# Optimization experiments

Measured on AMD Instinct MI355X. Metric: run time of the kernel, lower is better.

The kernel has to match this reference:

```python
import jax, jax.numpy as jnp
import numpy as np


def setup_inputs() -> dict:
    key = jax.random.key(0)
    k1, k2, k3 = jax.random.split(key, 3)
    Q, N, D = 2048, 100000, 512
    x = jax.random.normal(k1, (Q, D), dtype=jnp.float32)
    target_embeddings = jax.random.normal(k2, (N, D), dtype=jnp.float32)
    target_labels = jax.random.randint(k3, (N,), 0, 400, dtype=jnp.int64)
    return {"x": x, "target_embeddings": target_embeddings,
            "target_labels": target_labels, "k": 5}


def reference(x, target_embeddings, target_labels, k):
    # torch.cdist(x[:,None], T[None], p=2).squeeze(1): full [Q, N] euclidean distances
    x2 = jnp.sum(x * x, axis=-1, keepdims=True)            # [Q, 1]
    t2 = jnp.sum(target_embeddings * target_embeddings, axis=-1)  # [N]
    d2 = x2 + t2[None, :] - 2.0 * (x @ target_embeddings.T)       # [Q, N]
    dist = jnp.sqrt(jnp.maximum(d2, 0.0))
    # topk smallest distances
    neg_vals, topk_inds = jax.lax.top_k(-dist, k)           # [Q, k]
    topk_dists = -neg_vals
    # pred = target_labels[inds].t() in the original eval path
    pred = target_labels[topk_inds].T                       # [k, Q]
    return topk_dists, topk_inds, pred
```

## Files before the change

### kernel.cpp

```cpp
#include <hip/hip_runtime.h>
#include <hip/hip_fp8.h>
#include <float.h>
#include <math.h>

#define NQ 2048
#define NT 100000
#define DIM 512
#define KTOP 5
#define NCAND 16
#define QTILE 128
#define TTILE 128
#define NTPC 13
#define NCH 64
#define TBLKS 782
#define QBLKS 16
#define NSUB 3
#define CV_TBLKS (TBLKS*16)
#define CV_XBLKS ((NQ/128)*16)

typedef float f32x4 __attribute__((ext_vector_type(4)));
typedef unsigned int u32;
typedef unsigned short u16;
typedef unsigned long u64;

__device__ __forceinline__ int tsub_start(int ts) { return (13 * ts + 2) / 3; }

__device__ __forceinline__ bool lt_pair(float v1, int i1, float v2, int i2) {
  return v1 < v2 || (v1 == v2 && i1 < i2);
}

__device__ __forceinline__ void ins5f(float* tv, int* tix, float sc, int idx) {
  if (sc < tv[4]) {
    tv[4] = sc; tix[4] = idx;
#pragma unroll
    for (int p = 4; p > 0; --p)
      if (tv[p] < tv[p - 1]) {
        float tf = tv[p]; tv[p] = tv[p - 1]; tv[p - 1] = tf;
        int tn = tix[p]; tix[p] = tix[p - 1]; tix[p - 1] = tn;
      }
  }
}

__device__ __forceinline__ void ins5(float* tv, int* tix, float sc, int idx) {
  if (lt_pair(sc, idx, tv[4], tix[4])) {
    tv[4] = sc; tix[4] = idx;
#pragma unroll
    for (int p = 4; p > 0; --p)
      if (lt_pair(tv[p], tix[p], tv[p - 1], tix[p - 1])) {
        float tf = tv[p]; tv[p] = tv[p - 1]; tv[p - 1] = tf;
        int tn = tix[p]; tix[p] = tix[p - 1]; tix[p - 1] = tn;
      }
  }
}

__device__ __forceinline__ void merge5(float* av, int* ai, const float* bv, const int* bi) {
  float nv[5]; int ni[5];
#pragma unroll
  for (int s = 0; s < 5; ++s) {
    if (lt_pair(av[s], ai[s], bv[4 - s], bi[4 - s])) { nv[s] = av[s]; ni[s] = ai[s]; }
    else { nv[s] = bv[4 - s]; ni[s] = bi[4 - s]; }
  }
#pragma unroll
  for (int a = 0; a < 5; ++a)
#pragma unroll
    for (int b = 0; b < 4 - a; ++b)
      if (lt_pair(nv[b + 1], ni[b + 1], nv[b], ni[b])) {
        float tf = nv[b]; nv[b] = nv[b + 1]; nv[b + 1] = tf;
        int tn = ni[b]; ni[b] = ni[b + 1]; ni[b + 1] = tn;
      }
#pragma unroll
  for (int s = 0; s < 5; ++s) { av[s] = nv[s]; ai[s] = ni[s]; }
}

__global__ __launch_bounds__(256) void convert_kernel(
    const float* __restrict__ x, const float* __restrict__ T,
    unsigned char* __restrict__ xq8, unsigned char* __restrict__ tq8,
    float* __restrict__ t2, float* __restrict__ x2) {
  __shared__ unsigned char lh[4096];
  const int bid = blockIdx.x;
  const bool isT = bid < CV_TBLKS;
  const int task = isT ? bid : bid - CV_TBLKS;
  const int blk = task >> 4, kbi = task & 15;
  const float* src = isT ? T : x;
  unsigned char* dq8 = isT ? tq8 : xq8;
  float* nrm = isT ? t2 : x2;
  const int nsrc = isT ? NT : NQ;

  const int t = threadIdx.x;
  const int rr = t >> 1, half = t & 1;
  const int grow = blk * 128 + rr;
  const int rs = grow < nsrc ? grow : nsrc - 1;
  const float* p = src + (size_t)rs * DIM + kbi * 32 + half * 16;
  f32x4 v[4];
#pragma unroll
  for (int i = 0; i < 4; ++i) v[i] = ((const f32x4*)p)[i];

  float ss = 0.f;
#pragma unroll
  for (int g = 0; g < 2; ++g) {
    u64 pk = 0;
#pragma unroll
    for (int e = 0; e < 8; ++e) {
      int i = g * 8 + e;
      float f = v[i >> 2][i & 3];
      ss = fmaf(f, f, ss);
      __hip_fp8_e4m3 q8(f);
      pk |= (u64)__builtin_bit_cast(unsigned char, q8) << (8 * e);
    }
    int unit = (rr >> 4) * 64 + (half * 2 + g) * 16 + (rr & 15);
    *(u64*)(lh + unit * 8) = pk;
  }
  ss += __shfl_xor(ss, 1, 64);
  if (half == 0 && grow < nsrc) atomicAdd(nrm + grow, ss);

  __syncthreads();
  size_t obase = ((size_t)(blk * 16 + kbi)) * 4096 + t * 16;
  *(f32x4*)(dq8 + obase) = *(const f32x4*)(lh + t * 16);
}

__global__ __launch_bounds__(256, 2) void knn_mfma(
    const unsigned char* __restrict__ xq8, const unsigned char* __restrict__ tq8,
    const float* __restrict__ t2g,
    float* __restrict__ pvals, u16* __restrict__ pidx16) {
  __shared__ float msv[128 * 5];
  __shared__ int   msi[128 * 5];

  const int tid = threadIdx.x;
  const int w = tid >> 6;
  const int l = tid & 63;
  const int bid = blockIdx.x;
  const u32 rest = (u32)bid >> 3;
  const int inner = (int)(rest % 48u);
  const int chunk = (bid & 7) + 8 * (int)(rest / 48u);
  const int qblk = inner & 15;
  const int tsub = inner >> 4;
  const int tstart = tsub_start(tsub);
  const int tend = tsub_start(tsub + 1);
  const int q0 = qblk * QTILE;
  const int wr = (w >> 1) * 64;
  const int wc = (w & 1) * 64;
  const int arow = wr >> 4;
  const int bcol = wc >> 4;

  const u64* x64 = (const u64*)xq8;
  const u64* t64 = (const u64*)tq8;

  float tv4[4][KTOP]; int tix4[4][KTOP];
#pragma unroll
  for (int jj = 0; jj < 4; ++jj)
#pragma unroll
    for (int s = 0; s < KTOP; ++s) { tv4[jj][s] = FLT_MAX; tix4[jj][s] = 0x7FFFFFFF; }

#pragma unroll 1
  for (int tt = tstart; tt < tend; ++tt) {
    const int bblk = chunk * NTPC + tt;
    if (bblk >= TBLKS) continue;
    const int tbase = bblk * TTILE;
    f32x4 acc[4][4];
#pragma unroll
    for (int i = 0; i < 4; ++i)
#pragma unroll
      for (int j = 0; j < 4; ++j) acc[i][j] = (f32x4){0.f, 0.f, 0.f, 0.f};

    u32 offA = (u32)(bblk * 16) * 512u + (u32)(arow * 64 + l);
    u32 offB = (u32)(qblk * 16) * 512u + (u32)(bcol * 64 + l);
    long ah[4], bh[4];
#pragma unroll 1
    for (int kbi = 0; kbi < 16; ++kbi) {
#pragma unroll
      for (int i = 0; i < 4; ++i) {
        ah[i] = (long)t64[offA + i * 64];
        bh[i] = (long)x64[offB + i * 64];
      }
      offA += 512; offB += 512;
      __builtin_amdgcn_s_setprio(1);
#pragma unroll
      for (int j = 0; j < 4; ++j)
#pragma unroll
        for (int i = 0; i < 4; ++i)
          acc[i][j] = __builtin_amdgcn_mfma_f32_16x16x32_fp8_fp8(ah[i], bh[j], acc[i][j], 0, 0, 0);
      __builtin_amdgcn_s_setprio(0);
    }

    const int tg0 = tbase + wr + ((l >> 4) << 2);
    float t2v[16];
#pragma unroll
    for (int i = 0; i < 4; ++i)
#pragma unroll
      for (int r = 0; r < 4; ++r) {
        int t = tg0 + i * 16 + r;
        float vv = t2g[t < NT ? t : NT - 1];
        t2v[i * 4 + r] = t < NT ? vv : FLT_MAX;
      }
#pragma unroll
    for (int jj = 0; jj < 4; ++jj)
#pragma unroll
      for (int i = 0; i < 4; ++i)
#pragma unroll
        for (int r = 0; r < 4; ++r) {
          float sc = fmaf(-2.f, acc[i][jj][r], t2v[i * 4 + r]);
          ins5f(tv4[jj], tix4[jj], sc, tg0 + i * 16 + r);
        }
  }

#pragma unroll
  for (int jj = 0; jj < 4; ++jj)
#pragma unroll
    for (int d = 16; d <= 32; d <<= 1) {
      float ov[KTOP]; int oi[KTOP];
#pragma unroll
      for (int s = 0; s < KTOP; ++s) {
        ov[s] = __shfl_xor(tv4[jj][s], d, 64);
        oi[s] = __shfl_xor(tix4[jj][s], d, 64);
      }
      merge5(tv4[jj], tix4[jj], ov, oi);
    }

  const int blockBase = (chunk * NTPC + tstart) * TTILE;
  if ((w >> 1) && (l >> 4) == 0) {
#pragma unroll
    for (int jj = 0; jj < 4; ++jj) {
      int qr = wc + jj * 16 + l;
#pragma unroll
      for (int s = 0; s < KTOP; ++s) {
        msv[qr * 5 + s] = tv4[jj][s];
        msi[qr * 5 + s] = tix4[jj][s];
      }
    }
  }
  __syncthreads();
  if (!(w >> 1) && (l >> 4) == 0) {
#pragma unroll
    for (int jj = 0; jj < 4; ++jj) {
      int qr = wc + jj * 16 + l;
      float ov[KTOP]; int oi[KTOP];
#pragma unroll
      for (int s = 0; s < KTOP; ++s) { ov[s] = msv[qr * 5 + s]; oi[s] = msi[qr * 5 + s]; }
      merge5(tv4[jj], tix4[jj], ov, oi);
      int q = q0 + qr;
      size_t base = ((size_t)q * (NCH * NSUB) + (chunk * NSUB + tsub)) * KTOP;
#pragma unroll
      for (int s = 0; s < KTOP; ++s) {
        pvals[base + s] = tv4[jj][s];
        pidx16[base + s] = (u16)(tix4[jj][s] - blockBase);
      }
    }
  }
}

__global__ __launch_bounds__(256) void knn_merge16(
    const float* __restrict__ pvals, const u16* __restrict__ pidx16,
    int* __restrict__ idx16g) {
  const int M = NCH * NSUB * KTOP;
  int q = (blockIdx.x * 256 + threadIdx.x) >> 6;
  int l = threadIdx.x & 63;
  if (q >= NQ) return;
  float v[15]; int ix[15];
  size_t base = (size_t)q * M;
#pragma unroll
  for (int j = 0; j < 15; ++j) {
    int m = j * 64 + l;
    int slot = m / KTOP;
    int ch = slot / NSUB, ts = slot % NSUB;
    int gb = (ch * NTPC + tsub_start(ts)) * TTILE;
    v[j] = pvals[base + m];
    ix[j] = gb + (int)pidx16[base + m];
  }
  int mywin = 0x7FFFFFFF;
#pragma unroll 1
  for (int r = 0; r < NCAND; ++r) {
    float bv = FLT_MAX; int bi = 0x7FFFFFFF;
#pragma unroll
    for (int j = 0; j < 15; ++j)
      if (lt_pair(v[j], ix[j], bv, bi)) { bv = v[j]; bi = ix[j]; }
#pragma unroll
    for (int d = 1; d < 64; d <<= 1) {
      float ov = __shfl_xor(bv, d, 64);
      int oi = __shfl_xor(bi, d, 64);
      if (lt_pair(ov, oi, bv, bi)) { bv = ov; bi = oi; }
    }
    if (l == r) mywin = bi;
#pragma unroll
    for (int j = 0; j < 15; ++j)
      if (ix[j] == bi) v[j] = FLT_MAX;
  }
  if (l < NCAND) idx16g[q * NCAND + l] = mywin;
}

__global__ __launch_bounds__(256) void knn_rerank(
    const float* __restrict__ x, const float* __restrict__ T,
    const int* __restrict__ idx16g, const int* __restrict__ labels,
    float* __restrict__ out) {
  __shared__ float sd2[4 * NCAND];
  __shared__ int sti[4 * NCAND];
  const int w = threadIdx.x >> 6, l = threadIdx.x & 63;
  const int q = blockIdx.x * 4 + w;
  const int cand = l >> 2, sub = l & 3;
  const int ti = idx16g[q * NCAND + cand];
  const f32x4* tp = (const f32x4*)(T + (size_t)ti * DIM + sub * 128);
  const f32x4* xp = (const f32x4*)(x + (size_t)q * DIM + sub * 128);
  float dot = 0.f, tt = 0.f, xx = 0.f;
#pragma unroll
  for (int i = 0; i < 32; ++i) {
    f32x4 a = xp[i], b = tp[i];
#pragma unroll
    for (int c = 0; c < 4; ++c) {
      dot = fmaf(a[c], b[c], dot);
      tt  = fmaf(b[c], b[c], tt);
      xx  = fmaf(a[c], a[c], xx);
    }
  }
#pragma unroll
  for (int d = 1; d < 4; d <<= 1) {
    dot += __shfl_xor(dot, d, 64);
    tt  += __shfl_xor(tt, d, 64);
    xx  += __shfl_xor(xx, d, 64);
  }
  if (sub == 0) { sd2[w * NCAND + cand] = xx + tt - 2.f * dot; sti[w * NCAND + cand] = ti; }
  __syncthreads();
  if (l == 0) {
    float tv[KTOP]; int tix[KTOP];
#pragma unroll
    for (int s = 0; s < KTOP; ++s) { tv[s] = FLT_MAX; tix[s] = 0x7FFFFFFF; }
#pragma unroll
    for (int c = 0; c < NCAND; ++c) ins5(tv, tix, sd2[w * NCAND + c], sti[w * NCAND + c]);
#pragma unroll
    for (int s = 0; s < KTOP; ++s) {
      float d2 = tv[s] > 0.f ? tv[s] : 0.f;
      out[(size_t)q * KTOP + s] = sqrtf(d2);
      out[(size_t)NQ * KTOP + (size_t)q * KTOP + s] = (float)tix[s];
      out[(size_t)2 * NQ * KTOP + (size_t)s * NQ + q] =
          (float)labels[tix[s]];
    }
  }
}

extern "C" void kernel_launch(void* const* d_in, const int* in_sizes, int n_in,
                              void* d_out, int out_size, void* d_ws, size_t ws_size,
                              hipStream_t stream) {
  const float* x = (const float*)d_in[0];
  const float* T = (const float*)d_in[1];
  const int* labels = (const int*)d_in[2];
  float* out = (float*)d_out;
  char* ws = (char*)d_ws;

  float* t2     = (float*)(ws + 0);
  float* x2     = (float*)(ws + 401408);
  unsigned char* xq8 = (unsigned char*)(ws + 409600);
  unsigned char* tq8 = (unsigned char*)(ws + 1458176);
  float* pvals  = (float*)(ws + 52707328);
  u16*   pidx16 = (u16*)(ws + 60571648);
  int*   idx16g = (int*)(ws + 64503808);

  hipMemsetAsync(ws, 0, 409600, stream);

  convert_kernel<<<CV_TBLKS + CV_XBLKS, 256, 0, stream>>>(
      x, T, xq8, tq8, t2, x2);

  knn_mfma<<<QBLKS * NSUB * NCH, 256, 0, stream>>>(
      xq8, tq8, t2, pvals, pidx16);

  knn_merge16<<<(NQ * 64 + 255) / 256, 256, 0, stream>>>(pvals, pidx16, idx16g);

  knn_rerank<<<NQ / 4, 256, 0, stream>>>(x, T, idx16g, labels, out);
}
```

Baseline: 665.6 us.

## Repack FP8 operands in 16-byte units and load two k-slices per iteration

The convert kernel now packs each row's FP8 data in pairs of 32-element k-blocks, so each lane owns 16 contiguous bytes instead of 8. The GEMM loop issues one 128-bit load per operand per step and runs two MFMAs per load, halving the number of global load instructions and loop iterations. This costs more live registers per iteration and doubles the convert kernel's per-block LDS and work.

After: 609.5 us. 8.4% less time.

```diff
diff --git a/kernel.cpp b/kernel.cpp
--- a/kernel.cpp
+++ b/kernel.cpp
@@ -15,10 +15,11 @@
 #define TBLKS 782
 #define QBLKS 16
 #define NSUB 3
-#define CV_TBLKS (TBLKS*16)
-#define CV_XBLKS ((NQ/128)*16)
+#define CVP_TBLKS (TBLKS*8)
+#define CVP_XBLKS (QBLKS*8)
 
 typedef float f32x4 __attribute__((ext_vector_type(4)));
+typedef long lg2 __attribute__((ext_vector_type(2)));
 typedef unsigned int u32;
 typedef unsigned short u16;
 typedef unsigned long u64;
@@ -76,11 +77,11 @@
     const float* __restrict__ x, const float* __restrict__ T,
     unsigned char* __restrict__ xq8, unsigned char* __restrict__ tq8,
     float* __restrict__ t2, float* __restrict__ x2) {
-  __shared__ unsigned char lh[4096];
+  __shared__ unsigned char lh[8192];
   const int bid = blockIdx.x;
-  const bool isT = bid < CV_TBLKS;
-  const int task = isT ? bid : bid - CV_TBLKS;
-  const int blk = task >> 4, kbi = task & 15;
+  const bool isT = bid < CVP_TBLKS;
+  const int task = isT ? bid : bid - CVP_TBLKS;
+  const int blk = task >> 3, pair = task & 7;
   const float* src = isT ? T : x;
   unsigned char* dq8 = isT ? tq8 : xq8;
   float* nrm = isT ? t2 : x2;
@@ -90,14 +91,14 @@
   const int rr = t >> 1, half = t & 1;
   const int grow = blk * 128 + rr;
   const int rs = grow < nsrc ? grow : nsrc - 1;
-  const float* p = src + (size_t)rs * DIM + kbi * 32 + half * 16;
-  f32x4 v[4];
-#pragma unroll
-  for (int i = 0; i < 4; ++i) v[i] = ((const f32x4*)p)[i];
+  const float* p = src + (size_t)rs * DIM + pair * 64 + half * 32;
+  f32x4 v[8];
+#pragma unroll
+  for (int i = 0; i < 8; ++i) v[i] = ((const f32x4*)p)[i];
 
   float ss = 0.f;
 #pragma unroll
-  for (int g = 0; g < 2; ++g) {
+  for (int g = 0; g < 4; ++g) {
     u64 pk = 0;
 #pragma unroll
     for (int e = 0; e < 8; ++e) {
@@ -107,15 +108,16 @@
       __hip_fp8_e4m3 q8(f);
       pk |= (u64)__builtin_bit_cast(unsigned char, q8) << (8 * e);
     }
-    int unit = (rr >> 4) * 64 + (half * 2 + g) * 16 + (rr & 15);
-    *(u64*)(lh + unit * 8) = pk;
+    int unit = (rr >> 4) * 64 + g * 16 + (rr & 15);
+    *(u64*)(lh + unit * 16 + half * 8) = pk;
   }
   ss += __shfl_xor(ss, 1, 64);
   if (half == 0 && grow < nsrc) atomicAdd(nrm + grow, ss);
 
   __syncthreads();
-  size_t obase = ((size_t)(blk * 16 + kbi)) * 4096 + t * 16;
-  *(f32x4*)(dq8 + obase) = *(const f32x4*)(lh + t * 16);
+  size_t obase = ((size_t)(blk * 8 + pair)) * 8192 + t * 32;
+  *(f32x4*)(dq8 + obase)      = *(const f32x4*)(lh + t * 32);
+  *(f32x4*)(dq8 + obase + 16) = *(const f32x4*)(lh + t * 32 + 16);
 }
 
 __global__ __launch_bounds__(256, 2) void knn_mfma(
@@ -142,8 +144,8 @@
   const int arow = wr >> 4;
   const int bcol = wc >> 4;
 
-  const u64* x64 = (const u64*)xq8;
-  const u64* t64 = (const u64*)tq8;
+  const f32x4* x16 = (const f32x4*)xq8;
+  const f32x4* t16 = (const f32x4*)tq8;
 
   float tv4[4][KTOP]; int tix4[4][KTOP];
 #pragma unroll
@@ -162,23 +164,28 @@
 #pragma unroll
       for (int j = 0; j < 4; ++j) acc[i][j] = (f32x4){0.f, 0.f, 0.f, 0.f};
 
-    u32 offA = (u32)(bblk * 16) * 512u + (u32)(arow * 64 + l);
-    u32 offB = (u32)(qblk * 16) * 512u + (u32)(bcol * 64 + l);
-    long ah[4], bh[4];
+    u32 offA = (u32)(bblk * 8) * 512u + (u32)(arow * 64 + l);
+    u32 offB = (u32)(qblk * 8) * 512u + (u32)(bcol * 64 + l);
 #pragma unroll 1
-    for (int kbi = 0; kbi < 16; ++kbi) {
+    for (int p = 0; p < 8; ++p) {
+      f32x4 a2[4], b2[4];
 #pragma unroll
       for (int i = 0; i < 4; ++i) {
-        ah[i] = (long)t64[offA + i * 64];
-        bh[i] = (long)x64[offB + i * 64];
+        a2[i] = t16[offA + i * 64];
+        b2[i] = x16[offB + i * 64];
       }
       offA += 512; offB += 512;
       __builtin_amdgcn_s_setprio(1);
 #pragma unroll
-      for (int j = 0; j < 4; ++j)
-#pragma unroll
-        for (int i = 0; i < 4; ++i)
-          acc[i][j] = __builtin_amdgcn_mfma_f32_16x16x32_fp8_fp8(ah[i], bh[j], acc[i][j], 0, 0, 0);
+      for (int j = 0; j < 4; ++j) {
+        const lg2 bb = __builtin_bit_cast(lg2, b2[j]);
+#pragma unroll
+        for (int i = 0; i < 4; ++i) {
+          const lg2 aa = __builtin_bit_cast(lg2, a2[i]);
+          acc[i][j] = __builtin_amdgcn_mfma_f32_16x16x32_fp8_fp8(aa[0], bb[0], acc[i][j], 0, 0, 0);
+          acc[i][j] = __builtin_amdgcn_mfma_f32_16x16x32_fp8_fp8(aa[1], bb[1], acc[i][j], 0, 0, 0);
+        }
+      }
       __builtin_amdgcn_s_setprio(0);
     }
 
@@ -354,7 +361,7 @@
 
   hipMemsetAsync(ws, 0, 409600, stream);
 
-  convert_kernel<<<CV_TBLKS + CV_XBLKS, 256, 0, stream>>>(
+  convert_kernel<<<CVP_TBLKS + CVP_XBLKS, 256, 0, stream>>>(
       x, T, xq8, tq8, t2, x2);
 
   knn_mfma<<<QBLKS * NSUB * NCH, 256, 0, stream>>>(
```
